# Kernel tuning notes

Hardware: AMD Instinct MI355X
Metric: run time of the kernel (lower is better)

## Reference

```python
import jax, jax.numpy as jnp
import numpy as np

G_NUMS = 30      # group_nums
G_SIZE = 100     # group_size (also neighborhood_size)
BETA = 1.0
EPS = 1e-9


def setup_inputs() -> dict:
    key = jax.random.key(0)
    pointclouds = jax.random.normal(key, (8, 131072, 3), dtype=jnp.float32)
    return {"pointclouds": pointclouds}


def _knn_gather(points, queries, k):
    """points [b,N,3], queries [b,G,3] -> k nearest points per query [b,G,k,3]."""
    # squared distances [b,G,N]
    d2 = (
        jnp.sum(queries * queries, axis=-1)[..., None]
        - 2.0 * jnp.einsum("bgd,bnd->bgn", queries, points)
        + jnp.sum(points * points, axis=-1)[:, None, :]
    )
    _, idx = jax.lax.top_k(-d2, k)                    # [b,G,k]
    nbrs = jax.vmap(lambda p, i: p[i])(points, idx)   # [b,G,k,3]
    return nbrs


def reference(pointclouds):
    b, N, _ = pointclouds.shape
    # --- group_points: uniform-stride sampled centers, k-NN groups, group means ---
    stride = N // G_NUMS
    centers = pointclouds[:, ::stride][:, :G_NUMS]                 # [b,G,3]
    grouped = _knn_gather(pointclouds, centers, G_SIZE)            # [b,G,K,3]
    group_means = jnp.mean(grouped, axis=2)                        # [b,G,3]

    # --- estimate_pointcloud_local_coord_frames: per-group 3x3 PCA ---
    nbrs = _knn_gather(pointclouds, group_means, G_SIZE)           # [b,G,K,3]
    mu = jnp.mean(nbrs, axis=2, keepdims=True)
    X = nbrs - mu
    cov = jnp.einsum("bgkd,bgke->bgde", X, X) / G_SIZE             # [b,G,3,3]
    curvatures, frames = jnp.linalg.eigh(cov)                      # eigvals ascending

    # --- elongated-shape loss ---
    denom = curvatures[..., 0] + curvatures[..., 1] + curvatures[..., 2] + EPS
    first_vec = curvatures[..., 2] / denom
    second_vec = curvatures[..., 1] / denom
    elongated_shape_loss = -jnp.sum(first_vec - second_vec) / b

    # --- angular smoothness cost over group means / principal directions ---
    dirs = frames[..., :, 2]                                       # [b,G,3] largest-eig direction
    dm = jnp.sum(
        (group_means[:, :, None, :] - group_means[:, None, :, :]) ** 2, axis=-1
    )                                                              # [b,G,G]
    dm = dm + jnp.eye(G_NUMS, dtype=dm.dtype) * jnp.float32(1e30)  # exclude self
    j = jnp.argmin(dm, axis=-1)                                    # [b,G]
    dirs_j = jnp.take_along_axis(dirs, j[..., None], axis=1)       # [b,G,3]
    cos = jnp.sum(dirs * dirs_j, axis=-1)
    dlo_smooth_loss = jnp.mean(1.0 - cos * cos)                    # sign-invariant angle cost

    return elongated_shape_loss + BETA * dlo_smooth_loss
```

## Files before the change

### kernel.cpp

```cpp
#include <hip/hip_runtime.h>
#include <math.h>

#define N_PTS     131072
#define G_NUMS    30
#define G_SIZE    100
#define PT_STRIDE (N_PTS / G_NUMS)
#define TPB       1024
#define NWAVES    (TPB / 64)
#define BINS      4096
#define JB        (BINS / TPB)
#define SHIFT     20
#define SAMPLE_GRPS 1024
#define RANK_CUT  32
#define CAP       3072
#define TIE_CAP   64
#define SMP_N     2048
#define SMP_PL    (SMP_N / 64)
#define SMP_CUT   12
#define SMP_ITERS 13

struct KSmem {
    union {
        unsigned hist[BINS];
        struct {
            float gm[256][3];
            float dir[256][3];
            float pe[NWAVES];
            float ps[NWAVES];
        } fin;
    };
    unsigned wsum[NWAVES];
    unsigned T;
    int ns, nd, nt;
    unsigned u[CAP];
    int idx[CAP];
    float px[CAP], py[CAP], pz[CAP];
    int sel[G_SIZE];
    unsigned tu[TIE_CAP];
    int ti[TIE_CAP];
    float acc[3], cov[6], q[3];
    unsigned tau0, maxu, r1;
    float delta2;
};

__device__ __forceinline__ float dist2f(float px, float py, float pz,
                                        float qx, float qy, float qz) {
    float dx = px - qx, dy = py - qy, dz = pz - qz;
    return fmaf(dx, dx, fmaf(dy, dy, dz * dz));
}

__device__ __forceinline__ unsigned find_bin(KSmem& sm, unsigned rank,
                                             int tid, int lane, int wid) {
    unsigned hv[JB], csum = 0;
#pragma unroll
    for (int j = 0; j < JB; j++) { hv[j] = sm.hist[tid * JB + j]; csum += hv[j]; }
    unsigned inc = csum;
#pragma unroll
    for (int off = 1; off < 64; off <<= 1) {
        unsigned n = __shfl_up(inc, off);
        if (lane >= off) inc += n;
    }
    __syncthreads();
    if (lane == 63) sm.wsum[wid] = inc;
    __syncthreads();
    unsigned base = 0;
    for (int w = 0; w < wid; w++) base += sm.wsum[w];
    unsigned c = base + inc - csum;
#pragma unroll
    for (int j = 0; j < JB; j++) {
        if (c < rank && c + hv[j] >= rank) sm.T = (unsigned)(tid * JB + j);
        c += hv[j];
    }
    __syncthreads();
    return sm.T;
}

__device__ void fine_select(KSmem& sm, unsigned ubound, int tid, int lane, int wid) {
    int S = sm.ns; if (S > CAP) S = CAP;
    unsigned hb = 32u - (unsigned)__clz(ubound | 1u);
    unsigned s2 = hb > 12u ? hb - 12u : 0u;
    for (int i = tid; i < S; i += TPB) {
        unsigned bin = sm.u[i] >> s2; if (bin > BINS - 1u) bin = BINS - 1u;
        atomicAdd(&sm.hist[bin], 1u);
    }
    __syncthreads();
    unsigned T2 = find_bin(sm, G_SIZE, tid, lane, wid);
    for (int i = tid; i < S; i += TPB) {
        unsigned uu = sm.u[i];
        unsigned bin = uu >> s2; if (bin > BINS - 1u) bin = BINS - 1u;
        if (bin < T2) {
            int p = atomicAdd(&sm.nd, 1);
            if (p < G_SIZE) sm.sel[p] = i;
        } else if (bin == T2) {
            int p = atomicAdd(&sm.nt, 1);
            if (p < TIE_CAP) { sm.tu[p] = uu; sm.ti[p] = i; }
        }
    }
    __syncthreads();
    if (tid == 0) {
        int nd = sm.nd; if (nd > G_SIZE) nd = G_SIZE;
        int need = G_SIZE - nd;
        int ec = sm.nt; if (ec > TIE_CAP) ec = TIE_CAP;
        for (int a = 0; a < need && a < ec; ++a) {
            int best = a;
            for (int j = a + 1; j < ec; ++j)
                if (sm.tu[j] < sm.tu[best] ||
                    (sm.tu[j] == sm.tu[best] && sm.idx[sm.ti[j]] < sm.idx[sm.ti[best]])) best = j;
            unsigned tub = sm.tu[best]; sm.tu[best] = sm.tu[a]; sm.tu[a] = tub;
            int tib = sm.ti[best]; sm.ti[best] = sm.ti[a]; sm.ti[a] = tib;
            sm.sel[nd + a] = sm.ti[a];
        }
    }
    __syncthreads();
}

__device__ __forceinline__ void push4(KSmem& sm, const float4& xv, const float4& yv,
                                      const float4& zv, int i, unsigned tau,
                                      float qx, float qy, float qz) {
    unsigned u0 = __float_as_uint(dist2f(xv.x, yv.x, zv.x, qx, qy, qz));
    unsigned u1 = __float_as_uint(dist2f(xv.y, yv.y, zv.y, qx, qy, qz));
    unsigned u2 = __float_as_uint(dist2f(xv.z, yv.z, zv.z, qx, qy, qz));
    unsigned u3 = __float_as_uint(dist2f(xv.w, yv.w, zv.w, qx, qy, qz));
    int i0 = i * 4;
    if (u0 < tau) { int p = atomicAdd(&sm.ns, 1); if (p < CAP) { sm.u[p] = u0; sm.idx[p] = i0;     sm.px[p] = xv.x; sm.py[p] = yv.x; sm.pz[p] = zv.x; } }
    if (u1 < tau) { int p = atomicAdd(&sm.ns, 1); if (p < CAP) { sm.u[p] = u1; sm.idx[p] = i0 + 1; sm.px[p] = xv.y; sm.py[p] = yv.y; sm.pz[p] = zv.y; } }
    if (u2 < tau) { int p = atomicAdd(&sm.ns, 1); if (p < CAP) { sm.u[p] = u2; sm.idx[p] = i0 + 2; sm.px[p] = xv.z; sm.py[p] = yv.z; sm.pz[p] = zv.z; } }
    if (u3 < tau) { int p = atomicAdd(&sm.ns, 1); if (p < CAP) { sm.u[p] = u3; sm.idx[p] = i0 + 3; sm.px[p] = xv.w; sm.py[p] = yv.w; sm.pz[p] = zv.w; } }
}

__device__ void filter_exact(const float4* __restrict__ P4, KSmem& sm, unsigned tau,
                             float qx, float qy, float qz, int tid) {
    if (tid == 0) sm.ns = 0;
    __syncthreads();
#pragma unroll 4
    for (int grp = tid; grp < N_PTS / 4; grp += TPB) {
        float4 f0 = P4[3 * grp + 0];
        float4 f1 = P4[3 * grp + 1];
        float4 f2 = P4[3 * grp + 2];
        float4 xv = make_float4(f0.x, f0.w, f1.z, f2.y);
        float4 yv = make_float4(f0.y, f1.x, f1.w, f2.z);
        float4 zv = make_float4(f0.z, f1.y, f2.x, f2.w);
        push4(sm, xv, yv, zv, grp, tau, qx, qy, qz);
    }
    __syncthreads();
}

__device__ unsigned sample_tau(const float4* __restrict__ P4, KSmem& sm,
                               float qx, float qy, float qz,
                               int tid, int lane, int wid) {
    for (int j = tid; j < BINS; j += TPB) sm.hist[j] = 0u;
    if (tid == 0) { sm.ns = 0; sm.nd = 0; sm.nt = 0; sm.T = 0u; }
    __syncthreads();
    for (int grp = tid; grp < SAMPLE_GRPS; grp += TPB) {
        float4 f0 = P4[3 * grp + 0];
        float4 f1 = P4[3 * grp + 1];
        float4 f2 = P4[3 * grp + 2];
        atomicAdd(&sm.hist[__float_as_uint(dist2f(f0.x, f0.y, f0.z, qx, qy, qz)) >> SHIFT], 1u);
        atomicAdd(&sm.hist[__float_as_uint(dist2f(f0.w, f1.x, f1.y, qx, qy, qz)) >> SHIFT], 1u);
        atomicAdd(&sm.hist[__float_as_uint(dist2f(f1.z, f1.w, f2.x, qx, qy, qz)) >> SHIFT], 1u);
        atomicAdd(&sm.hist[__float_as_uint(dist2f(f2.y, f2.z, f2.w, qx, qy, qz)) >> SHIFT], 1u);
    }
    __syncthreads();
    unsigned Tc = find_bin(sm, RANK_CUT, tid, lane, wid);
    unsigned tau = (Tc >= BINS - 1) ? 0xFFFFFFFFu : ((Tc + 1) << SHIFT);
    for (int j = tid; j < BINS; j += TPB) sm.hist[j] = 0u;
    __syncthreads();
    return tau;
}

__device__ void knn_exact(const float4* __restrict__ P4, KSmem& sm,
                          float qx, float qy, float qz,
                          int tid, int lane, int wid, bool save_tau) {
    unsigned tau = sample_tau(P4, sm, qx, qy, qz, tid, lane, wid);
    if (save_tau && tid == 0) sm.tau0 = tau;
    filter_exact(P4, sm, tau, qx, qy, qz, tid);
    fine_select(sm, tau, tid, lane, wid);
}

__device__ void eig3(const float cf[6], double lam_out[3], double dir_out[3]) {
    double a[3][3], v[3][3];
    a[0][0] = cf[0]; a[0][1] = cf[1]; a[0][2] = cf[2];
    a[1][0] = cf[1]; a[1][1] = cf[3]; a[1][2] = cf[4];
    a[2][0] = cf[2]; a[2][1] = cf[4]; a[2][2] = cf[5];
    for (int i = 0; i < 3; i++)
        for (int j = 0; j < 3; j++) v[i][j] = (i == j) ? 1.0 : 0.0;
    for (int sweep = 0; sweep < 12; sweep++) {
        double off = a[0][1] * a[0][1] + a[0][2] * a[0][2] + a[1][2] * a[1][2];
        if (off == 0.0) break;
        for (int p = 0; p < 2; p++) {
            for (int q = p + 1; q < 3; q++) {
                double apq = a[p][q];
                if (apq == 0.0) continue;
                double app = a[p][p], aqq = a[q][q];
                double theta = (aqq - app) / (2.0 * apq);
                double t = (theta >= 0.0 ? 1.0 : -1.0) /
                           (fabs(theta) + sqrt(theta * theta + 1.0));
                double c = 1.0 / sqrt(t * t + 1.0);
                double s = t * c;
                a[p][p] = app - t * apq;
                a[q][q] = aqq + t * apq;
                a[p][q] = 0.0; a[q][p] = 0.0;
                for (int r = 0; r < 3; r++) {
                    if (r == p || r == q) continue;
                    double arp = a[r][p], arq = a[r][q];
                    a[r][p] = c * arp - s * arq; a[p][r] = a[r][p];
                    a[r][q] = s * arp + c * arq; a[q][r] = a[r][q];
                }
                for (int r = 0; r < 3; r++) {
                    double vrp = v[r][p], vrq = v[r][q];
                    v[r][p] = c * vrp - s * vrq;
                    v[r][q] = s * vrp + c * vrq;
                }
            }
        }
    }
    double l0 = a[0][0], l1 = a[1][1], l2 = a[2][2];
    int i0 = 0, i1 = 1, i2 = 2;
    if (l0 > l1) { double t = l0; l0 = l1; l1 = t; int ti = i0; i0 = i1; i1 = ti; }
    if (l1 > l2) { double t = l1; l1 = l2; l2 = t; int ti = i1; i1 = i2; i2 = ti; }
    if (l0 > l1) { double t = l0; l0 = l1; l1 = t; int ti = i0; i0 = i1; i1 = ti; }
    lam_out[0] = l0; lam_out[1] = l1; lam_out[2] = l2;
    dir_out[0] = v[0][i2]; dir_out[1] = v[1][i2]; dir_out[2] = v[2][i2];
}

__global__ __launch_bounds__(TPB)
void fused_knn_kernel(const float* __restrict__ pts,
                      float* __restrict__ gmeans, float* __restrict__ covs,
                      float* __restrict__ out,
                      unsigned* __restrict__ syncw,
                      int B, int nblk) {
    __shared__ KSmem sm;
    __shared__ int s_fastok;
    __shared__ int s_last;

    const int blk = blockIdx.x;
    const int b = blk % B;
    const int g = blk / B;
    const int gi = b * G_NUMS + g;
    const float* __restrict__ P = pts + (size_t)b * (N_PTS * 3);
    const float4* __restrict__ P4 = (const float4*)P;
    const int tid = threadIdx.x;
    const int lane = tid & 63, wid = tid >> 6;

    if (tid == 0) {
        const float* qp = P + (size_t)g * PT_STRIDE * 3;
        sm.q[0] = qp[0]; sm.q[1] = qp[1]; sm.q[2] = qp[2];
        sm.ns = 0; sm.nd = 0; sm.nt = 0; sm.T = 0u;
        s_last = 0;
    }
    if (tid < 3) sm.acc[tid] = 0.f;
    if (tid < 6) sm.cov[tid] = 0.f;
    for (int j = tid; j < BINS; j += TPB) sm.hist[j] = 0u;
    for (int t = tid; t < SMP_N / 4; t += TPB) {
        float4 f0 = P4[3 * t + 0];
        float4 f1 = P4[3 * t + 1];
        float4 f2 = P4[3 * t + 2];
        sm.px[4 * t + 0] = f0.x; sm.px[4 * t + 1] = f0.w;
        sm.px[4 * t + 2] = f1.z; sm.px[4 * t + 3] = f2.y;
        sm.py[4 * t + 0] = f0.y; sm.py[4 * t + 1] = f1.x;
        sm.py[4 * t + 2] = f1.w; sm.py[4 * t + 3] = f2.z;
        sm.pz[4 * t + 0] = f0.z; sm.pz[4 * t + 1] = f1.y;
        sm.pz[4 * t + 2] = f2.x; sm.pz[4 * t + 3] = f2.w;
    }
    __syncthreads();
    const float qx = sm.q[0], qy = sm.q[1], qz = sm.q[2];

    unsigned tau;
    {
        unsigned du[SMP_PL];
#pragma unroll
        for (int k = 0; k < SMP_PL; ++k) {
            int p = lane + 64 * k;
            du[k] = __float_as_uint(dist2f(sm.px[p], sm.py[p], sm.pz[p], qx, qy, qz));
        }
        unsigned lo = 0u, hi = 0x7F800000u;
        for (int it = 0; it < SMP_ITERS; ++it) {
            unsigned mid = (lo + hi) >> 1;
            int cnt = 0;
#pragma unroll
            for (int k = 0; k < SMP_PL; ++k) cnt += (du[k] < mid) ? 1 : 0;
#pragma unroll
            for (int off = 1; off < 64; off <<= 1) cnt += __shfl_xor(cnt, off);
            if (cnt >= SMP_CUT) hi = mid; else lo = mid;
        }
        tau = hi;
    }
    __syncthreads();
    if (tid == 0) sm.tau0 = tau;

    filter_exact(P4, sm, tau, qx, qy, qz, tid);
    int S0 = sm.ns;
    bool anomaly = (S0 < G_SIZE) || (S0 > CAP);
    if (anomaly) {
        knn_exact(P4, sm, qx, qy, qz, tid, lane, wid, true);
    } else {
        fine_select(sm, tau, tid, lane, wid);
    }

    if (tid < G_SIZE) {
        int p = sm.sel[tid];
        atomicAdd(&sm.acc[0], sm.px[p]);
        atomicAdd(&sm.acc[1], sm.py[p]);
        atomicAdd(&sm.acc[2], sm.pz[p]);
    }
    __syncthreads();
    S0 = sm.ns;
    if (tid == 0) {
        float mx = sm.acc[0] * (1.0f / G_SIZE);
        float my = sm.acc[1] * (1.0f / G_SIZE);
        float mz = sm.acc[2] * (1.0f / G_SIZE);
        gmeans[(size_t)gi * 3 + 0] = mx;
        gmeans[(size_t)gi * 3 + 1] = my;
        gmeans[(size_t)gi * 3 + 2] = mz;
        float dx = mx - qx, dy = my - qy, dz = mz - qz;
        sm.delta2 = fmaf(dx, dx, fmaf(dy, dy, dz * dz));
        sm.q[0] = mx; sm.q[1] = my; sm.q[2] = mz;
        sm.acc[0] = 0.f; sm.acc[1] = 0.f; sm.acc[2] = 0.f;
        sm.maxu = 0u; sm.r1 = 0u; sm.T = 0u;
        sm.nd = 0; sm.nt = 0;
        s_fastok = 0;
    }
    __syncthreads();
    const float q1x = sm.q[0], q1y = sm.q[1], q1z = sm.q[2];

    const bool attempt = (S0 >= G_SIZE) && (S0 <= CAP);
    if (attempt) {
        for (int j = tid; j < BINS; j += TPB) sm.hist[j] = 0u;
        for (int i = tid; i < S0; i += TPB) {
            unsigned uu = __float_as_uint(
                dist2f(sm.px[i], sm.py[i], sm.pz[i], q1x, q1y, q1z));
            sm.u[i] = uu;
            atomicMax(&sm.maxu, uu);
        }
        __syncthreads();
        unsigned maxu = sm.maxu;
        unsigned hb = (maxu == 0u) ? 0u : (32u - (unsigned)__clz(maxu));
        unsigned s3 = hb > 12u ? hb - 12u : 0u;
        for (int i = tid; i < S0; i += TPB) atomicAdd(&sm.hist[sm.u[i] >> s3], 1u);
        __syncthreads();
        unsigned T2 = find_bin(sm, G_SIZE, tid, lane, wid);
        const unsigned lo = T2 << s3;
        for (int i = tid; i < S0; i += TPB) {
            unsigned uu = sm.u[i];
            if (uu < lo) {
                int p = atomicAdd(&sm.nd, 1);
                if (p < G_SIZE) sm.sel[p] = i;
            } else if ((uu >> s3) == T2) {
                int p = atomicAdd(&sm.nt, 1);
                if (p < TIE_CAP) { sm.tu[p] = uu; sm.ti[p] = i; }
            }
        }
        __syncthreads();
        if (tid == 0) {
            int ok = 1;
            int nd = sm.nd; if (nd > G_SIZE) { nd = G_SIZE; ok = 0; }
            int need = G_SIZE - nd;
            if (sm.nt > TIE_CAP) ok = 0;
            int ec = sm.nt; if (ec > TIE_CAP) ec = TIE_CAP;
            if (need > ec) ok = 0;
            for (int a = 0; a < need && a < ec; ++a) {
                int best = a;
                for (int j = a + 1; j < ec; ++j)
                    if (sm.tu[j] < sm.tu[best] ||
                        (sm.tu[j] == sm.tu[best] && sm.idx[sm.ti[j]] < sm.idx[sm.ti[best]])) best = j;
                unsigned tub = sm.tu[best]; sm.tu[best] = sm.tu[a]; sm.tu[a] = tub;
                int tib = sm.ti[best]; sm.ti[best] = sm.ti[a]; sm.ti[a] = tib;
                sm.sel[nd + a] = sm.ti[a];
            }
            s_fastok = ok;
        }
        __syncthreads();
        if (s_fastok) {
            if (tid < G_SIZE) atomicMax(&sm.r1, sm.u[sm.sel[tid]]);
            __syncthreads();
            if (tid == 0) {
                double R0 = sqrt((double)__uint_as_float(sm.tau0));
                double dl = sqrt((double)sm.delta2);
                double r1 = sqrt((double)__uint_as_float(sm.r1));
                if (!((R0 - dl) > r1 * 1.0001 + 1e-7)) s_fastok = 0;
            }
            __syncthreads();
        }
    }

    if (!attempt || !s_fastok) {
        knn_exact(P4, sm, q1x, q1y, q1z, tid, lane, wid, false);
    }

    float px = 0.f, py = 0.f, pz = 0.f;
    if (tid < G_SIZE) {
        int p = sm.sel[tid];
        px = sm.px[p]; py = sm.py[p]; pz = sm.pz[p];
        atomicAdd(&sm.acc[0], px);
        atomicAdd(&sm.acc[1], py);
        atomicAdd(&sm.acc[2], pz);
    }
    __syncthreads();
    float mx = sm.acc[0] * (1.0f / G_SIZE);
    float my = sm.acc[1] * (1.0f / G_SIZE);
    float mz = sm.acc[2] * (1.0f / G_SIZE);
    if (tid < G_SIZE) {
        float x = px - mx, y = py - my, z = pz - mz;
        atomicAdd(&sm.cov[0], x * x);
        atomicAdd(&sm.cov[1], x * y);
        atomicAdd(&sm.cov[2], x * z);
        atomicAdd(&sm.cov[3], y * y);
        atomicAdd(&sm.cov[4], y * z);
        atomicAdd(&sm.cov[5], z * z);
    }
    __syncthreads();
    if (tid < 6) covs[(size_t)gi * 6 + tid] = sm.cov[tid] * (1.0f / G_SIZE);

    __syncthreads();
    if (tid == 0) {
        unsigned old = __hip_atomic_fetch_add(&syncw[0], 1u, __ATOMIC_RELEASE,
                                              __HIP_MEMORY_SCOPE_AGENT);
        s_last = (old == (unsigned)(nblk - 1)) ? 1 : 0;
    }
    __syncthreads();
    if (!s_last) return;

    (void)__hip_atomic_load(&syncw[0], __ATOMIC_ACQUIRE, __HIP_MEMORY_SCOPE_AGENT);
    const int NG = nblk;
    float et = 0.f;
    if (tid < NG) {
        float cf[6];
#pragma unroll
        for (int j = 0; j < 6; j++) cf[j] = covs[tid * 6 + j];
        double lam[3], dir[3];
        eig3(cf, lam, dir);
        double denom = lam[0] + lam[1] + lam[2] + 1e-9;
        et = (float)((lam[2] - lam[1]) / denom);
        sm.fin.dir[tid][0] = (float)dir[0];
        sm.fin.dir[tid][1] = (float)dir[1];
        sm.fin.dir[tid][2] = (float)dir[2];
        sm.fin.gm[tid][0] = gmeans[tid * 3 + 0];
        sm.fin.gm[tid][1] = gmeans[tid * 3 + 1];
        sm.fin.gm[tid][2] = gmeans[tid * 3 + 2];
    }
    __syncthreads();

    float st = 0.f;
    if (tid < NG) {
        int bb = tid / G_NUMS, gg0 = tid % G_NUMS;
        float gx = sm.fin.gm[tid][0], gy = sm.fin.gm[tid][1], gz = sm.fin.gm[tid][2];
        float bd = 3.4e38f; int bj = 0;
        for (int gg = 0; gg < G_NUMS; gg++) {
            if (gg == gg0) continue;
            int o = bb * G_NUMS + gg;
            float dx = gx - sm.fin.gm[o][0];
            float dy = gy - sm.fin.gm[o][1];
            float dz = gz - sm.fin.gm[o][2];
            float d = dx * dx + dy * dy + dz * dz;
            if (d < bd) { bd = d; bj = gg; }
        }
        int o = bb * G_NUMS + bj;
        float cosv = sm.fin.dir[tid][0] * sm.fin.dir[o][0] +
                     sm.fin.dir[tid][1] * sm.fin.dir[o][1] +
                     sm.fin.dir[tid][2] * sm.fin.dir[o][2];
        st = 1.f - cosv * cosv;
    }

    float e = et, s2v = st;
#pragma unroll
    for (int off = 32; off > 0; off >>= 1) {
        e += __shfl_down(e, off);
        s2v += __shfl_down(s2v, off);
    }
    if (lane == 0) { sm.fin.pe[wid] = e; sm.fin.ps[wid] = s2v; }
    __syncthreads();
    if (tid == 0) {
        float se = 0.f, ss = 0.f;
        for (int w = 0; w < NWAVES; w++) { se += sm.fin.pe[w]; ss += sm.fin.ps[w]; }
        out[0] = -se / (float)B + ss / (float)NG;
    }
}

extern "C" void kernel_launch(void* const* d_in, const int* in_sizes, int n_in,
                              void* d_out, int out_size, void* d_ws, size_t ws_size,
                              hipStream_t stream) {
    const float* pts = (const float*)d_in[0];
    float* out = (float*)d_out;
    float* ws = (float*)d_ws;
    int B = in_sizes[0] / (N_PTS * 3);
    int nblk = B * G_NUMS;

    float* gmeans = ws;
    float* covs = ws + (size_t)3 * nblk;
    unsigned* syncw = (unsigned*)(ws + (size_t)9 * nblk);

    hipMemsetAsync(syncw, 0, 64, stream);

    fused_knn_kernel<<<dim3(nblk), dim3(TPB), 0, stream>>>(
        pts, gmeans, covs, out, syncw, B, nblk);
}
```

Baseline: 146.8 us.

## Quantize points to 16-bit SoA planes for the first kNN filter pass

Adds a preprocessing kernel that quantizes every point into 16-bit fixed-point x/y/z planes and flags any values outside the representable range. The first kNN pass then streams these compact planes instead of the float AoS data. It uses a conservatively widened threshold to collect candidates, recomputes exact distances on the gathered originals, and checks the result, falling back to the exact path on any doubt. The aim is to cut the memory traffic of the full-cloud scan. In exchange it adds an extra launch and a full pass that reads the float data and writes the planes. The second kNN stage is unchanged, and the quantized path only runs if the workspace is large enough.

Result: slower. 151.2 us (+3.0%).

```diff
diff --git a/kernel.cpp b/kernel.cpp
--- a/kernel.cpp
+++ b/kernel.cpp
@@ -15,9 +15,12 @@
 #define CAP       3072
 #define TIE_CAP   64
 #define SMP_N     2048
-#define SMP_PL    (SMP_N / 64)
+#define SMP_PL    32
 #define SMP_CUT   12
 #define SMP_ITERS 13
+#define QS16      (1.0f / 4096.0f)
+#define QC16      (-8.0f + 0.5f / 4096.0f)
+#define QM16      3.0e-4f
 
 struct KSmem {
     union {
@@ -175,6 +178,21 @@
     if (save_tau && tid == 0) sm.tau0 = tau;
     filter_exact(P4, sm, tau, qx, qy, qz, tid);
     fine_select(sm, tau, tid, lane, wid);
+}
+
+__device__ __forceinline__ void q16filt2(KSmem& sm, unsigned xw, unsigned yw,
+                                         unsigned zw, int i0, float tauf,
+                                         float Cx, float Cy, float Cz) {
+    float dx0 = fmaf((float)(xw & 0xffffu), QS16, Cx);
+    float dy0 = fmaf((float)(yw & 0xffffu), QS16, Cy);
+    float dz0 = fmaf((float)(zw & 0xffffu), QS16, Cz);
+    float d0 = fmaf(dx0, dx0, fmaf(dy0, dy0, dz0 * dz0));
+    float dx1 = fmaf((float)(xw >> 16), QS16, Cx);
+    float dy1 = fmaf((float)(yw >> 16), QS16, Cy);
+    float dz1 = fmaf((float)(zw >> 16), QS16, Cz);
+    float d1 = fmaf(dx1, dx1, fmaf(dy1, dy1, dz1 * dz1));
+    if (d0 < tauf) { int p = atomicAdd(&sm.ns, 1); if (p < CAP) sm.idx[p] = i0; }
+    if (d1 < tauf) { int p = atomicAdd(&sm.ns, 1); if (p < CAP) sm.idx[p] = i0 + 1; }
 }
 
 __device__ void eig3(const float cf[6], double lam_out[3], double dir_out[3]) {
@@ -223,15 +241,18 @@
     dir_out[0] = v[0][i2]; dir_out[1] = v[1][i2]; dir_out[2] = v[2][i2];
 }
 
+template<int MODE>
 __global__ __launch_bounds__(TPB)
 void fused_knn_kernel(const float* __restrict__ pts,
+                      const unsigned short* __restrict__ xq,
+                      const unsigned short* __restrict__ yq,
+                      const unsigned short* __restrict__ zq,
                       float* __restrict__ gmeans, float* __restrict__ covs,
                       float* __restrict__ out,
                       unsigned* __restrict__ syncw,
                       int B, int nblk) {
     __shared__ KSmem sm;
-    __shared__ int s_fastok;
-    __shared__ int s_last;
+    __shared__ int s_fastok, s_last, s_exact, s_chk;
 
     const int blk = blockIdx.x;
     const int b = blk % B;
@@ -239,6 +260,12 @@
     const int gi = b * G_NUMS + g;
     const float* __restrict__ P = pts + (size_t)b * (N_PTS * 3);
     const float4* __restrict__ P4 = (const float4*)P;
+    const unsigned* XW = nullptr; const unsigned* YW = nullptr; const unsigned* ZW = nullptr;
+    if (MODE == 1) {
+        XW = (const unsigned*)(xq + (size_t)b * N_PTS);
+        YW = (const unsigned*)(yq + (size_t)b * N_PTS);
+        ZW = (const unsigned*)(zq + (size_t)b * N_PTS);
+    }
     const int tid = threadIdx.x;
     const int lane = tid & 63, wid = tid >> 6;
 
@@ -247,54 +274,91 @@
         sm.q[0] = qp[0]; sm.q[1] = qp[1]; sm.q[2] = qp[2];
         sm.ns = 0; sm.nd = 0; sm.nt = 0; sm.T = 0u;
         s_last = 0;
+        s_exact = (MODE == 0) ? 1 : (syncw[1] ? 1 : 0);
     }
     if (tid < 3) sm.acc[tid] = 0.f;
     if (tid < 6) sm.cov[tid] = 0.f;
     for (int j = tid; j < BINS; j += TPB) sm.hist[j] = 0u;
-    for (int t = tid; t < SMP_N / 4; t += TPB) {
-        float4 f0 = P4[3 * t + 0];
-        float4 f1 = P4[3 * t + 1];
-        float4 f2 = P4[3 * t + 2];
-        sm.px[4 * t + 0] = f0.x; sm.px[4 * t + 1] = f0.w;
-        sm.px[4 * t + 2] = f1.z; sm.px[4 * t + 3] = f2.y;
-        sm.py[4 * t + 0] = f0.y; sm.py[4 * t + 1] = f1.x;
-        sm.py[4 * t + 2] = f1.w; sm.py[4 * t + 3] = f2.z;
-        sm.pz[4 * t + 0] = f0.z; sm.pz[4 * t + 1] = f1.y;
-        sm.pz[4 * t + 2] = f2.x; sm.pz[4 * t + 3] = f2.w;
-    }
     __syncthreads();
     const float qx = sm.q[0], qy = sm.q[1], qz = sm.q[2];
 
-    unsigned tau;
-    {
-        unsigned du[SMP_PL];
-#pragma unroll
-        for (int k = 0; k < SMP_PL; ++k) {
-            int p = lane + 64 * k;
-            du[k] = __float_as_uint(dist2f(sm.px[p], sm.py[p], sm.pz[p], qx, qy, qz));
-        }
-        unsigned lo = 0u, hi = 0x7F800000u;
-        for (int it = 0; it < SMP_ITERS; ++it) {
-            unsigned mid = (lo + hi) >> 1;
-            int cnt = 0;
-#pragma unroll
-            for (int k = 0; k < SMP_PL; ++k) cnt += (du[k] < mid) ? 1 : 0;
-#pragma unroll
-            for (int off = 1; off < 64; off <<= 1) cnt += __shfl_xor(cnt, off);
-            if (cnt >= SMP_CUT) hi = mid; else lo = mid;
-        }
-        tau = hi;
-    }
-    __syncthreads();
-    if (tid == 0) sm.tau0 = tau;
-
-    filter_exact(P4, sm, tau, qx, qy, qz, tid);
-    int S0 = sm.ns;
-    bool anomaly = (S0 < G_SIZE) || (S0 > CAP);
-    if (anomaly) {
+    if (s_exact) {
         knn_exact(P4, sm, qx, qy, qz, tid, lane, wid, true);
     } else {
-        fine_select(sm, tau, tid, lane, wid);
+        const float Cx = QC16 - qx, Cy = QC16 - qy, Cz = QC16 - qz;
+        unsigned tau_q;
+        {
+            unsigned du[SMP_PL];
+#pragma unroll
+            for (int k = 0; k < SMP_PL / 2; ++k) {
+                int w = lane + 64 * k;
+                unsigned xw = XW[w], yw = YW[w], zw = ZW[w];
+                float dx0 = fmaf((float)(xw & 0xffffu), QS16, Cx);
+                float dy0 = fmaf((float)(yw & 0xffffu), QS16, Cy);
+                float dz0 = fmaf((float)(zw & 0xffffu), QS16, Cz);
+                du[2 * k] = __float_as_uint(fmaf(dx0, dx0, fmaf(dy0, dy0, dz0 * dz0)));
+                float dx1 = fmaf((float)(xw >> 16), QS16, Cx);
+                float dy1 = fmaf((float)(yw >> 16), QS16, Cy);
+                float dz1 = fmaf((float)(zw >> 16), QS16, Cz);
+                du[2 * k + 1] = __float_as_uint(fmaf(dx1, dx1, fmaf(dy1, dy1, dz1 * dz1)));
+            }
+            unsigned lo = 0u, hi = 0x7F800000u;
+            for (int it = 0; it < SMP_ITERS; ++it) {
+                unsigned mid = (lo + hi) >> 1;
+                int cnt = 0;
+#pragma unroll
+                for (int k = 0; k < SMP_PL; ++k) cnt += (du[k] < mid) ? 1 : 0;
+#pragma unroll
+                for (int off = 1; off < 64; off <<= 1) cnt += __shfl_xor(cnt, off);
+                if (cnt >= SMP_CUT) hi = mid; else lo = mid;
+            }
+            tau_q = hi;
+        }
+        const float t = sqrtf(__uint_as_float(tau_q));
+        const float tf = t + QM16;
+        const float tauf = tf * tf;
+        const float rm = t + 2.0f * QM16;
+        const unsigned umax = __float_as_uint(fmaf(rm, rm, 1e-6f) * 1.0001f);
+        if (tid == 0) { sm.tau0 = tau_q; sm.ns = 0; }
+        __syncthreads();
+
+        const uint4* XQ4 = (const uint4*)XW;
+        const uint4* YQ4 = (const uint4*)YW;
+        const uint4* ZQ4 = (const uint4*)ZW;
+#pragma unroll 4
+        for (int it = 0; it < N_PTS / 8 / TPB; ++it) {
+            int i = it * TPB + tid;
+            uint4 xv = XQ4[i], yv = YQ4[i], zv = ZQ4[i];
+            int i0 = i * 8;
+            q16filt2(sm, xv.x, yv.x, zv.x, i0 + 0, tauf, Cx, Cy, Cz);
+            q16filt2(sm, xv.y, yv.y, zv.y, i0 + 2, tauf, Cx, Cy, Cz);
+            q16filt2(sm, xv.z, yv.z, zv.z, i0 + 4, tauf, Cx, Cy, Cz);
+            q16filt2(sm, xv.w, yv.w, zv.w, i0 + 6, tauf, Cx, Cy, Cz);
+        }
+        __syncthreads();
+        int S = sm.ns;
+        if (S < G_SIZE || S > CAP) {
+            knn_exact(P4, sm, qx, qy, qz, tid, lane, wid, true);
+        } else {
+            for (int i = tid; i < S; i += TPB) {
+                const float* pp = P + 3 * (size_t)sm.idx[i];
+                float x = pp[0], y = pp[1], z = pp[2];
+                sm.px[i] = x; sm.py[i] = y; sm.pz[i] = z;
+                sm.u[i] = __float_as_uint(dist2f(x, y, z, qx, qy, qz));
+            }
+            __syncthreads();
+            fine_select(sm, umax, tid, lane, wid);
+            if (tid == 0) sm.maxu = 0u;
+            __syncthreads();
+            if (tid < G_SIZE) atomicMax(&sm.maxu, sm.u[sm.sel[tid]]);
+            __syncthreads();
+            if (tid == 0)
+                s_chk = (__uint_as_float(sm.maxu) < t * t * (1.0f - 1e-5f)) ? 1 : 0;
+            __syncthreads();
+            if (!s_chk) {
+                knn_exact(P4, sm, qx, qy, qz, tid, lane, wid, true);
+            }
+        }
     }
 
     if (tid < G_SIZE) {
@@ -304,7 +368,7 @@
         atomicAdd(&sm.acc[2], sm.pz[p]);
     }
     __syncthreads();
-    S0 = sm.ns;
+    const int S0 = sm.ns;
     if (tid == 0) {
         float mx = sm.acc[0] * (1.0f / G_SIZE);
         float my = sm.acc[1] * (1.0f / G_SIZE);
@@ -476,6 +540,41 @@
     }
 }
 
+__global__ __launch_bounds__(256)
+void quant16_kernel(const float* __restrict__ pts,
+                    unsigned short* __restrict__ xq, unsigned short* __restrict__ yq,
+                    unsigned short* __restrict__ zq, unsigned* __restrict__ syncw,
+                    int total4) {
+    int t = blockIdx.x * 256 + threadIdx.x;
+    if (t >= total4) return;
+    const float4* __restrict__ P4 = (const float4*)pts;
+    float4 f0 = P4[3 * t + 0];
+    float4 f1 = P4[3 * t + 1];
+    float4 f2 = P4[3 * t + 2];
+    float xs[4] = {f0.x, f0.w, f1.z, f2.y};
+    float ys[4] = {f0.y, f1.x, f1.w, f2.z};
+    float zs[4] = {f0.z, f1.y, f2.x, f2.w};
+    unsigned xw[2] = {0, 0}, yw[2] = {0, 0}, zw[2] = {0, 0};
+    int bad = 0;
+#pragma unroll
+    for (int j = 0; j < 4; ++j) {
+        int ix = (int)floorf((xs[j] + 8.0f) * 4096.0f);
+        int iy = (int)floorf((ys[j] + 8.0f) * 4096.0f);
+        int iz = (int)floorf((zs[j] + 8.0f) * 4096.0f);
+        if ((unsigned)ix > 65535u || (unsigned)iy > 65535u || (unsigned)iz > 65535u) bad = 1;
+        ix = ix < 0 ? 0 : (ix > 65535 ? 65535 : ix);
+        iy = iy < 0 ? 0 : (iy > 65535 ? 65535 : iy);
+        iz = iz < 0 ? 0 : (iz > 65535 ? 65535 : iz);
+        xw[j >> 1] |= (unsigned)ix << (16 * (j & 1));
+        yw[j >> 1] |= (unsigned)iy << (16 * (j & 1));
+        zw[j >> 1] |= (unsigned)iz << (16 * (j & 1));
+    }
+    ((uint2*)xq)[t] = make_uint2(xw[0], xw[1]);
+    ((uint2*)yq)[t] = make_uint2(yw[0], yw[1]);
+    ((uint2*)zq)[t] = make_uint2(zw[0], zw[1]);
+    if (bad) atomicOr(&syncw[1], 1u);
+}
+
 extern "C" void kernel_launch(void* const* d_in, const int* in_sizes, int n_in,
                               void* d_out, int out_size, void* d_ws, size_t ws_size,
                               hipStream_t stream) {
@@ -488,9 +587,26 @@
     float* gmeans = ws;
     float* covs = ws + (size_t)3 * nblk;
     unsigned* syncw = (unsigned*)(ws + (size_t)9 * nblk);
+    size_t plane_off = ((size_t)9 * nblk + 16) * 4;
+    plane_off = (plane_off + 15) & ~(size_t)15;
+    unsigned short* xqp = (unsigned short*)((char*)d_ws + plane_off);
+    size_t planeB = (size_t)B * N_PTS * 2;
+    unsigned short* yqp = (unsigned short*)((char*)xqp + planeB);
+    unsigned short* zqp = (unsigned short*)((char*)yqp + planeB);
+    size_t need = plane_off + 3 * planeB;
+    const int use_q = ws_size >= need;
 
     hipMemsetAsync(syncw, 0, 64, stream);
 
-    fused_knn_kernel<<<dim3(nblk), dim3(TPB), 0, stream>>>(
-        pts, gmeans, covs, out, syncw, B, nblk);
-}
+    dim3 grid(nblk);
+    if (use_q) {
+        int total4 = B * N_PTS / 4;
+        quant16_kernel<<<dim3((total4 + 255) / 256), dim3(256), 0, stream>>>(
+            pts, xqp, yqp, zqp, syncw, total4);
+        fused_knn_kernel<1><<<grid, dim3(TPB), 0, stream>>>(
+            pts, xqp, yqp, zqp, gmeans, covs, out, syncw, B, nblk);
+    } else {
+        fused_knn_kernel<0><<<grid, dim3(TPB), 0, stream>>>(
+            pts, nullptr, nullptr, nullptr, gmeans, covs, out, syncw, B, nblk);
+    }
+}
```
